# Performance work log

Hardware: AMD Instinct MI355X
Metric: run time of the kernel (lower is better)

The kernel has to match this reference:

```python
import jax, jax.numpy as jnp
import numpy as np

B = 8; R = 32; BS = 4; C = 128; H = 4; MLP = 512
SHIFT = BS // 2
N = BS ** 3            # tokens per window = 64
G = R // BS            # windows per axis = 8
NW = G ** 3            # windows per sample = 512
HD = C // H


def _rel_pos_index():
    # Faithful to the torch code: only coord 0 is scaled by (3*BS-1),
    # coords 1 and 2 are just added (index collisions are intentional here).
    coords = np.stack(np.meshgrid(np.arange(BS), np.arange(BS), np.arange(BS), indexing='ij'))
    cf = coords.reshape(3, -1)
    rel = (cf[:, :, None] - cf[:, None, :]).transpose(1, 2, 0).astype(np.int64)
    rel += BS - 1
    rel[:, :, 0] *= 3 * BS - 1
    return rel.sum(-1)  # (N, N)


def _attn_mask():
    img = np.zeros((R, R, R), np.float32)
    slices = (slice(0, -BS), slice(-BS, -SHIFT), slice(-SHIFT, None))
    cnt = 0
    for sx in slices:
        for sy in slices:
            for sz in slices:
                img[sx, sy, sz] = cnt
                cnt += 1
    boxes = img.reshape(G, BS, G, BS, G, BS).transpose(0, 2, 4, 1, 3, 5).reshape(-1, N)
    d = boxes[:, None, :] - boxes[:, :, None]  # (NW, N, N)
    return np.where(d != 0, np.float32(-100.0), np.float32(0.0))


_RPI = _rel_pos_index()
_MASK = _attn_mask()


def setup_inputs() -> dict:
    key = jax.random.key(0)
    ks = jax.random.split(key, 16)
    s = 0.02
    return {
        'inputs': jax.random.normal(ks[0], (B, R ** 3, C), jnp.float32),
        'qkv_w': jax.random.normal(ks[1], (C, 3 * C), jnp.float32) * s,
        'proj_w': jax.random.normal(ks[2], (C, C), jnp.float32) * s,
        'proj_b': jnp.zeros((C,), jnp.float32),
        'bias_table': jax.random.normal(ks[3], ((3 * BS - 1) ** 2, H), jnp.float32) * s,
        'g1': jnp.ones((C,), jnp.float32),
        'b1': jnp.zeros((C,), jnp.float32),
        'g2': jnp.ones((C,), jnp.float32),
        'b2': jnp.zeros((C,), jnp.float32),
        'w1': jax.random.normal(ks[4], (C, MLP), jnp.float32) * s,
        'bb1': jnp.zeros((MLP,), jnp.float32),
        'w2': jax.random.normal(ks[5], (MLP, C), jnp.float32) * s,
        'bb2': jnp.zeros((C,), jnp.float32),
    }


def _ln(x, g, b):
    m = x.mean(-1, keepdims=True)
    v = x.var(-1, keepdims=True)
    return (x - m) * jax.lax.rsqrt(v + 1e-5) * g + b


def reference(inputs, qkv_w, proj_w, proj_b, bias_table, g1, b1, g2, b2, w1, bb1, w2, bb2):
    rpi = jnp.asarray(_RPI)
    mask = jnp.asarray(_MASK)

    x = _ln(inputs, g1, b1).reshape(B, R, R, R, C)
    x = jnp.roll(x, (-SHIFT, -SHIFT, -SHIFT), axis=(1, 2, 3))
    # box partition -> (B*NW, N, C)
    boxes = x.reshape(B, G, BS, G, BS, G, BS, C).transpose(0, 1, 3, 5, 2, 4, 6, 7).reshape(-1, N, C)

    qkv = (boxes @ qkv_w).reshape(-1, N, 3, H, HD).transpose(2, 0, 3, 1, 4)
    q, k, v = qkv[0] * (HD ** -0.5), qkv[1], qkv[2]
    attn = jnp.einsum('bhnd,bhmd->bhnm', q, k)

    bias = bias_table[rpi.reshape(-1)].reshape(N, N, H).transpose(2, 0, 1)  # (H, N, N)
    attn = attn + bias[None]
    attn = attn.reshape(B, NW, H, N, N) + mask[None, :, None]
    attn = jax.nn.softmax(attn.reshape(-1, H, N, N), axis=-1)

    out = jnp.einsum('bhnm,bhmd->bhnd', attn, v).transpose(0, 2, 1, 3).reshape(-1, N, C)
    out = out @ proj_w + proj_b

    # box reverse + unshift
    out = out.reshape(B, G, G, G, BS, BS, BS, C).transpose(0, 1, 4, 2, 5, 3, 6, 7).reshape(B, R, R, R, C)
    out = jnp.roll(out, (SHIFT, SHIFT, SHIFT), axis=(1, 2, 3)).reshape(B, R ** 3, C)

    x = out * 0.5 + inputs
    h = _ln(x, g2, b2)
    h = jax.nn.gelu(h @ w1 + bb1, approximate=False) @ w2 + bb2
    return h * 0.5 + x
```

## Files before the change

kernel.cpp:

```cpp
#include <hip/hip_runtime.h>
#include <hip/hip_bf16.h>

typedef unsigned short u16;
typedef unsigned int u32;
typedef __attribute__((ext_vector_type(8))) short short8;
typedef __attribute__((ext_vector_type(4))) float f32x4;

__device__ __forceinline__ u16 f2bf(float x) {
  __hip_bfloat16 h = __float2bfloat16(x);
  return *reinterpret_cast<u16*>(&h);
}

__global__ void k_wprep(const float* __restrict__ src, u16* __restrict__ dst, int K, int N) {
  int idx = blockIdx.x * 256 + threadIdx.x;
  if (idx >= K * N) return;
  int k = idx / N, n = idx - k * N;
  dst[n * K + k] = f2bf(src[idx]);
}

__global__ __launch_bounds__(256, 2) void k_fused(const float* __restrict__ inputs,
                                                  const u16* __restrict__ qkvT,
                                                  const u16* __restrict__ projT,
                                                  const float* __restrict__ proj_b,
                                                  const float* __restrict__ btab,
                                                  const float* __restrict__ g1,
                                                  const float* __restrict__ b1,
                                                  float* __restrict__ xws) {
  __shared__ __align__(16) char lds[76800];
  u16* A_s  = (u16*)lds;
  u16* Q_s  = (u16*)(lds + 19456);
  u16* K_s  = (u16*)(lds + 36864);
  u16* P_s  = (u16*)lds;
  u16* O_s  = (u16*)(lds + 36864);
  u16* Vt_s = (u16*)(lds + 54272);
  float* bias_s = (float*)(lds + 72704);
  float* red    = (float*)(lds + 74752);

  const int t = threadIdx.x, wv = t >> 6, lane = t & 63;
  const int m = lane & 15, q4 = lane >> 4;
  const int bw = blockIdx.x;
  const int wbox = bw & 511, bsm = bw >> 9;
  const int gx = wbox >> 6, gy = (wbox >> 3) & 7, gz = wbox & 7;

  for (int i = t; i < 484; i += 256) bias_s[(i & 3) * 128 + (i >> 2)] = btab[i];

  short8 bq[4][2];
  #pragma unroll
  for (int kc = 0; kc < 4; ++kc)
    #pragma unroll
    for (int nt2 = 0; nt2 < 2; ++nt2)
      bq[kc][nt2] = *(const short8*)(qkvT + (size_t)(wv * 32 + nt2 * 16 + m) * 128 + kc * 32 + q4 * 8);

  {
    const int r1 = t >> 2, seg = t & 3;
    const int ix = r1 >> 4, iy = (r1 >> 2) & 3, iz = r1 & 3;
    const int X = (gx * 4 + ix + 2) & 31, Y = (gy * 4 + iy + 2) & 31, Z = (gz * 4 + iz + 2) & 31;
    const size_t orig = ((size_t)bsm << 15) + (size_t)(X * 1024 + Y * 32 + Z);
    const float4* x4 = (const float4*)(inputs + orig * 128 + seg * 32);
    float vals[32];
    float s = 0.f, ss = 0.f;
    #pragma unroll
    for (int i = 0; i < 8; ++i) {
      float4 v = x4[i];
      vals[4 * i] = v.x; vals[4 * i + 1] = v.y; vals[4 * i + 2] = v.z; vals[4 * i + 3] = v.w;
      s += v.x + v.y + v.z + v.w;
      ss += v.x * v.x + v.y * v.y + v.z * v.z + v.w * v.w;
    }
    red[r1 * 8 + seg] = s; red[r1 * 8 + 4 + seg] = ss;
    float sum = red[r1 * 8 + 0] + red[r1 * 8 + 1] + red[r1 * 8 + 2] + red[r1 * 8 + 3];
    float sq  = red[r1 * 8 + 4] + red[r1 * 8 + 5] + red[r1 * 8 + 6] + red[r1 * 8 + 7];
    float mean = sum * 0.0078125f;
    float var = sq * 0.0078125f - mean * mean;
    float rs = rsqrtf(var + 1e-5f);
    #pragma unroll
    for (int i = 0; i < 32; ++i) {
      int c = seg * 32 + i;
      A_s[r1 * 152 + c] = f2bf((vals[i] - mean) * rs * g1[c] + b1[c]);
    }
  }
  __syncthreads();

  short8 bk[4][2];
  #pragma unroll
  for (int kc = 0; kc < 4; ++kc)
    #pragma unroll
    for (int nt2 = 0; nt2 < 2; ++nt2)
      bk[kc][nt2] = *(const short8*)(qkvT + (size_t)(128 + wv * 32 + nt2 * 16 + m) * 128 + kc * 32 + q4 * 8);

  short8 af[4][4];
  #pragma unroll
  for (int kc = 0; kc < 4; ++kc)
    #pragma unroll
    for (int mt = 0; mt < 4; ++mt)
      af[kc][mt] = *(const short8*)(A_s + (mt * 16 + m) * 152 + kc * 32 + q4 * 8);

  f32x4 zero = {0.f, 0.f, 0.f, 0.f};

  {
    f32x4 acc1[4][2];
    #pragma unroll
    for (int mt = 0; mt < 4; ++mt)
      #pragma unroll
      for (int nt2 = 0; nt2 < 2; ++nt2) acc1[mt][nt2] = zero;
    #pragma unroll
    for (int kc = 0; kc < 4; ++kc)
      #pragma unroll
      for (int mt = 0; mt < 4; ++mt)
        #pragma unroll
        for (int nt2 = 0; nt2 < 2; ++nt2)
          acc1[mt][nt2] = __builtin_amdgcn_mfma_f32_16x16x32_bf16(af[kc][mt], bq[kc][nt2], acc1[mt][nt2], 0, 0, 0);
    #pragma unroll
    for (int mt = 0; mt < 4; ++mt)
      #pragma unroll
      for (int nt2 = 0; nt2 < 2; ++nt2)
        #pragma unroll
        for (int r = 0; r < 4; ++r)
          Q_s[(mt * 16 + q4 * 4 + r) * 136 + wv * 32 + nt2 * 16 + m] =
              f2bf(acc1[mt][nt2][r] * 0.17677669529663687f);
  }

  short8 bv[4][2];
  #pragma unroll
  for (int kc = 0; kc < 4; ++kc)
    #pragma unroll
    for (int nt2 = 0; nt2 < 2; ++nt2)
      bv[kc][nt2] = *(const short8*)(qkvT + (size_t)(256 + wv * 32 + nt2 * 16 + m) * 128 + kc * 32 + q4 * 8);

  {
    f32x4 acc1[4][2];
    #pragma unroll
    for (int mt = 0; mt < 4; ++mt)
      #pragma unroll
      for (int nt2 = 0; nt2 < 2; ++nt2) acc1[mt][nt2] = zero;
    #pragma unroll
    for (int kc = 0; kc < 4; ++kc)
      #pragma unroll
      for (int mt = 0; mt < 4; ++mt)
        #pragma unroll
        for (int nt2 = 0; nt2 < 2; ++nt2)
          acc1[mt][nt2] = __builtin_amdgcn_mfma_f32_16x16x32_bf16(af[kc][mt], bk[kc][nt2], acc1[mt][nt2], 0, 0, 0);
    #pragma unroll
    for (int mt = 0; mt < 4; ++mt)
      #pragma unroll
      for (int nt2 = 0; nt2 < 2; ++nt2)
        #pragma unroll
        for (int r = 0; r < 4; ++r)
          K_s[(mt * 16 + q4 * 4 + r) * 136 + wv * 32 + nt2 * 16 + m] = f2bf(acc1[mt][nt2][r]);
  }

  {
    f32x4 acc1[4][2];
    #pragma unroll
    for (int mt = 0; mt < 4; ++mt)
      #pragma unroll
      for (int nt2 = 0; nt2 < 2; ++nt2) acc1[mt][nt2] = zero;
    #pragma unroll
    for (int kc = 0; kc < 4; ++kc)
      #pragma unroll
      for (int mt = 0; mt < 4; ++mt)
        #pragma unroll
        for (int nt2 = 0; nt2 < 2; ++nt2)
          acc1[mt][nt2] = __builtin_amdgcn_mfma_f32_16x16x32_bf16(af[kc][mt], bv[kc][nt2], acc1[mt][nt2], 0, 0, 0);
    #pragma unroll
    for (int mt = 0; mt < 4; ++mt)
      #pragma unroll
      for (int nt2 = 0; nt2 < 2; ++nt2)
        #pragma unroll
        for (int r = 0; r < 4; ++r)
          Vt_s[wv * 2304 + (nt2 * 16 + m) * 72 + mt * 16 + q4 * 4 + r] = f2bf(acc1[mt][nt2][r]);
  }

  short8 qf[4], kf[4];
  #pragma unroll
  for (int ti = 0; ti < 4; ++ti) {
    qf[ti] = *(const short8*)(Q_s + (ti * 16 + m) * 136 + wv * 32 + q4 * 8);
    kf[ti] = *(const short8*)(K_s + (ti * 16 + m) * 136 + wv * 32 + q4 * 8);
  }
  __syncthreads();

  f32x4 S[4][4];
  #pragma unroll
  for (int ti = 0; ti < 4; ++ti)
    #pragma unroll
    for (int tj = 0; tj < 4; ++tj) S[ti][tj] = zero;
  #pragma unroll
  for (int ti = 0; ti < 4; ++ti)
    #pragma unroll
    for (int tj = 0; tj < 4; ++tj)
      S[ti][tj] = __builtin_amdgcn_mfma_f32_16x16x32_bf16(qf[ti], kf[tj], S[ti][tj], 0, 0, 0);

  int catx[4], caty[4], catz[4];
  #pragma unroll
  for (int a = 0; a < 4; ++a) {
    catx[a] = (gx < 7) ? 0 : ((a < 2) ? 1 : 2);
    caty[a] = (gy < 7) ? 0 : ((a < 2) ? 1 : 2);
    catz[a] = (gz < 7) ? 0 : ((a < 2) ? 1 : 2);
  }
  const int cy = (m >> 2) & 3, cz = m & 3;
  int labc[4], labr[16];
  #pragma unroll
  for (int tj = 0; tj < 4; ++tj) labc[tj] = catx[tj] * 9 + caty[cy] * 3 + catz[cz];
  #pragma unroll
  for (int ti = 0; ti < 4; ++ti)
    #pragma unroll
    for (int r = 0; r < 4; ++r) labr[ti * 4 + r] = catx[ti] * 9 + caty[q4] * 3 + catz[r];

  #pragma unroll
  for (int ti = 0; ti < 4; ++ti)
    #pragma unroll
    for (int tj = 0; tj < 4; ++tj) {
      int K0 = 11 * (ti - tj + 3) + (q4 + 3 - cy) + (3 - cz);
      #pragma unroll
      for (int r = 0; r < 4; ++r) {
        float v = S[ti][tj][r] + bias_s[wv * 128 + K0 + r];
        if (labr[ti * 4 + r] != labc[tj]) v -= 100.f;
        S[ti][tj][r] = v;
      }
    }

  float mx[16], sm[16];
  #pragma unroll
  for (int ti = 0; ti < 4; ++ti)
    #pragma unroll
    for (int r = 0; r < 4; ++r)
      mx[ti * 4 + r] = fmaxf(fmaxf(S[ti][0][r], S[ti][1][r]), fmaxf(S[ti][2][r], S[ti][3][r]));
  #pragma unroll
  for (int off = 1; off < 16; off <<= 1)
    #pragma unroll
    for (int i = 0; i < 16; ++i) mx[i] = fmaxf(mx[i], __shfl_xor(mx[i], off, 64));
  #pragma unroll
  for (int ti = 0; ti < 4; ++ti)
    #pragma unroll
    for (int r = 0; r < 4; ++r) {
      float e0 = __expf(S[ti][0][r] - mx[ti * 4 + r]);
      float e1 = __expf(S[ti][1][r] - mx[ti * 4 + r]);
      float e2 = __expf(S[ti][2][r] - mx[ti * 4 + r]);
      float e3 = __expf(S[ti][3][r] - mx[ti * 4 + r]);
      S[ti][0][r] = e0; S[ti][1][r] = e1; S[ti][2][r] = e2; S[ti][3][r] = e3;
      sm[ti * 4 + r] = (e0 + e1) + (e2 + e3);
    }
  #pragma unroll
  for (int off = 1; off < 16; off <<= 1)
    #pragma unroll
    for (int i = 0; i < 16; ++i) sm[i] += __shfl_xor(sm[i], off, 64);
  #pragma unroll
  for (int i = 0; i < 16; ++i) sm[i] = 1.f / sm[i];

  #pragma unroll
  for (int ti = 0; ti < 4; ++ti)
    #pragma unroll
    for (int tj = 0; tj < 4; ++tj)
      #pragma unroll
      for (int r = 0; r < 4; ++r)
        P_s[wv * 4608 + (ti * 16 + q4 * 4 + r) * 72 + tj * 16 + m] = f2bf(S[ti][tj][r]);

  f32x4 O[4][2];
  #pragma unroll
  for (int ti = 0; ti < 4; ++ti)
    #pragma unroll
    for (int tv = 0; tv < 2; ++tv) O[ti][tv] = zero;
  #pragma unroll
  for (int ks = 0; ks < 2; ++ks) {
    short8 pa[4], vb[2];
    #pragma unroll
    for (int ti = 0; ti < 4; ++ti)
      pa[ti] = *(const short8*)(P_s + wv * 4608 + (ti * 16 + m) * 72 + ks * 32 + q4 * 8);
    #pragma unroll
    for (int tv = 0; tv < 2; ++tv)
      vb[tv] = *(const short8*)(Vt_s + wv * 2304 + (tv * 16 + m) * 72 + ks * 32 + q4 * 8);
    #pragma unroll
    for (int ti = 0; ti < 4; ++ti)
      #pragma unroll
      for (int tv = 0; tv < 2; ++tv)
        O[ti][tv] = __builtin_amdgcn_mfma_f32_16x16x32_bf16(pa[ti], vb[tv], O[ti][tv], 0, 0, 0);
  }

  #pragma unroll
  for (int ti = 0; ti < 4; ++ti)
    #pragma unroll
    for (int tv = 0; tv < 2; ++tv)
      #pragma unroll
      for (int r = 0; r < 4; ++r)
        O_s[(ti * 16 + q4 * 4 + r) * 136 + wv * 32 + tv * 16 + m] = f2bf(O[ti][tv][r] * sm[ti * 4 + r]);

  short8 bp[4][2];
  #pragma unroll
  for (int kc = 0; kc < 4; ++kc)
    #pragma unroll
    for (int nt2 = 0; nt2 < 2; ++nt2)
      bp[kc][nt2] = *(const short8*)(projT + (size_t)(wv * 32 + nt2 * 16 + m) * 128 + kc * 32 + q4 * 8);
  float pb[2] = {proj_b[wv * 32 + m], proj_b[wv * 32 + 16 + m]};

  __syncthreads();

  short8 af2[4][4];
  #pragma unroll
  for (int kc = 0; kc < 4; ++kc)
    #pragma unroll
    for (int mt = 0; mt < 4; ++mt)
      af2[kc][mt] = *(const short8*)(O_s + (mt * 16 + m) * 136 + kc * 32 + q4 * 8);
  f32x4 acc2[4][2];
  #pragma unroll
  for (int mt = 0; mt < 4; ++mt)
    #pragma unroll
    for (int nt2 = 0; nt2 < 2; ++nt2) acc2[mt][nt2] = zero;
  #pragma unroll
  for (int kc = 0; kc < 4; ++kc)
    #pragma unroll
    for (int mt = 0; mt < 4; ++mt)
      #pragma unroll
      for (int nt2 = 0; nt2 < 2; ++nt2)
        acc2[mt][nt2] = __builtin_amdgcn_mfma_f32_16x16x32_bf16(af2[kc][mt], bp[kc][nt2], acc2[mt][nt2], 0, 0, 0);

  #pragma unroll
  for (int mt = 0; mt < 4; ++mt)
    #pragma unroll
    for (int r = 0; r < 4; ++r) {
      int nn = mt * 16 + q4 * 4 + r;
      int ix = nn >> 4, iy = (nn >> 2) & 3, iz = nn & 3;
      int X = (gx * 4 + ix + 2) & 31, Y = (gy * 4 + iy + 2) & 31, Z = (gz * 4 + iz + 2) & 31;
      size_t orig = ((size_t)bsm << 15) + (size_t)(X * 1024 + Y * 32 + Z);
      #pragma unroll
      for (int nt2 = 0; nt2 < 2; ++nt2) {
        int col = wv * 32 + nt2 * 16 + m;
        float v = acc2[mt][nt2][r] + pb[nt2];
        xws[orig * 128 + col] = 0.5f * v + inputs[orig * 128 + col];
      }
    }
}

__global__ __launch_bounds__(256, 2) void k_mlp(const float* __restrict__ x,
                                                const u16* __restrict__ w1T,
                                                const u16* __restrict__ w2T,
                                                const float* __restrict__ g2,
                                                const float* __restrict__ b2,
                                                const float* __restrict__ bb1,
                                                const float* __restrict__ bb2,
                                                float* __restrict__ out) {
  __shared__ __align__(16) char lds[19456];
  u16* A_s = (u16*)lds;
  float* red = (float*)(lds + 17408);
  u16* H0  = (u16*)lds;
  u16* H1  = (u16*)(lds + 9216);

  const int t = threadIdx.x, wid = t >> 6, lane = t & 63;
  const int m = lane & 15, q4 = lane >> 4;
  const size_t mbase = (size_t)blockIdx.x * 64;

  const u16* w1base = w1T + (size_t)(wid * 16 + m) * 128 + q4 * 8;
  short8 b1p0[4], b1p1[4];
  #pragma unroll
  for (int kc = 0; kc < 4; ++kc) b1p0[kc] = *(const short8*)(w1base + kc * 32);
  #pragma unroll
  for (int kc = 0; kc < 4; ++kc) b1p1[kc] = *(const short8*)(w1base + (size_t)64 * 128 + kc * 32);

  float bias1[8];
  #pragma unroll
  for (int nt = 0; nt < 8; ++nt) bias1[nt] = bb1[nt * 64 + wid * 16 + m];

  {
    int r1 = t >> 2, seg = t & 3;
    const float4* x4 = (const float4*)(x + (mbase + r1) * 128 + seg * 32);
    float vals[32];
    float s = 0.f, ss = 0.f;
    #pragma unroll
    for (int i = 0; i < 8; ++i) {
      float4 v = x4[i];
      vals[4 * i] = v.x; vals[4 * i + 1] = v.y; vals[4 * i + 2] = v.z; vals[4 * i + 3] = v.w;
      s += v.x + v.y + v.z + v.w;
      ss += v.x * v.x + v.y * v.y + v.z * v.z + v.w * v.w;
    }
    red[r1 * 8 + seg] = s; red[r1 * 8 + 4 + seg] = ss;
    float sum = red[r1 * 8 + 0] + red[r1 * 8 + 1] + red[r1 * 8 + 2] + red[r1 * 8 + 3];
    float sq  = red[r1 * 8 + 4] + red[r1 * 8 + 5] + red[r1 * 8 + 6] + red[r1 * 8 + 7];
    float mean = sum * 0.0078125f;
    float var = sq * 0.0078125f - mean * mean;
    float rs = rsqrtf(var + 1e-5f);
    #pragma unroll
    for (int i = 0; i < 32; ++i) {
      int c = seg * 32 + i;
      A_s[r1 * 136 + c] = f2bf((vals[i] - mean) * rs * g2[c] + b2[c]);
    }
  }
  __syncthreads();

  short8 af[4][4];
  #pragma unroll
  for (int kc = 0; kc < 4; ++kc)
    #pragma unroll
    for (int mt = 0; mt < 4; ++mt)
      af[kc][mt] = *(const short8*)(A_s + (mt * 16 + m) * 136 + kc * 32 + q4 * 8);
  __syncthreads();

  f32x4 zero = {0.f, 0.f, 0.f, 0.f};
  f32x4 acc[4][2];
  #pragma unroll
  for (int mt = 0; mt < 4; ++mt)
    #pragma unroll
    for (int nt2 = 0; nt2 < 2; ++nt2) acc[mt][nt2] = zero;

  #pragma unroll
  for (int nt = 0; nt < 8; ++nt) {
    u16* Hb = (nt & 1) ? H1 : H0;
    f32x4 hacc[4];
    #pragma unroll
    for (int mt = 0; mt < 4; ++mt) hacc[mt] = zero;
    if (nt & 1) {
      #pragma unroll
      for (int kc = 0; kc < 4; ++kc)
        #pragma unroll
        for (int mt = 0; mt < 4; ++mt)
          hacc[mt] = __builtin_amdgcn_mfma_f32_16x16x32_bf16(af[kc][mt], b1p1[kc], hacc[mt], 0, 0, 0);
    } else {
      #pragma unroll
      for (int kc = 0; kc < 4; ++kc)
        #pragma unroll
        for (int mt = 0; mt < 4; ++mt)
          hacc[mt] = __builtin_amdgcn_mfma_f32_16x16x32_bf16(af[kc][mt], b1p0[kc], hacc[mt], 0, 0, 0);
    }

    short8 b2f[2][2];
    #pragma unroll
    for (int kc2 = 0; kc2 < 2; ++kc2)
      #pragma unroll
      for (int nt2 = 0; nt2 < 2; ++nt2)
        b2f[kc2][nt2] = *(const short8*)(w2T + (size_t)(wid * 32 + nt2 * 16 + m) * 512 +
                                         nt * 64 + kc2 * 32 + q4 * 8);

    float bias = bias1[nt];
    #pragma unroll
    for (int mt = 0; mt < 4; ++mt)
      #pragma unroll
      for (int r = 0; r < 4; ++r) {
        float v = hacc[mt][r] + bias;
        float v2 = v * v;
        float qe = v * __builtin_fmaf(-0.07135482f, v2, -1.5957691f);
        float te = __expf(qe);
        float gl = v * __builtin_amdgcn_rcpf(1.f + te);
        Hb[(mt * 16 + q4 * 4 + r) * 72 + wid * 16 + m] = f2bf(gl);
      }
    __syncthreads();

    if (nt < 6) {
      const u16* p = w1base + (size_t)(nt + 2) * 64 * 128;
      if (nt & 1) {
        #pragma unroll
        for (int kc = 0; kc < 4; ++kc) b1p1[kc] = *(const short8*)(p + kc * 32);
      } else {
        #pragma unroll
        for (int kc = 0; kc < 4; ++kc) b1p0[kc] = *(const short8*)(p + kc * 32);
      }
    }

    #pragma unroll
    for (int kc2 = 0; kc2 < 2; ++kc2) {
      short8 a2[4];
      #pragma unroll
      for (int mt = 0; mt < 4; ++mt)
        a2[mt] = *(const short8*)(Hb + (mt * 16 + m) * 72 + kc2 * 32 + q4 * 8);
      #pragma unroll
      for (int mt = 0; mt < 4; ++mt)
        #pragma unroll
        for (int nt2 = 0; nt2 < 2; ++nt2)
          acc[mt][nt2] = __builtin_amdgcn_mfma_f32_16x16x32_bf16(a2[mt], b2f[kc2][nt2],
                                                                 acc[mt][nt2], 0, 0, 0);
    }
  }

  #pragma unroll
  for (int mt = 0; mt < 4; ++mt)
    #pragma unroll
    for (int nt2 = 0; nt2 < 2; ++nt2)
      #pragma unroll
      for (int r = 0; r < 4; ++r) {
        size_t tok = mbase + mt * 16 + q4 * 4 + r;
        int col = wid * 32 + nt2 * 16 + m;
        float v = acc[mt][nt2][r] + bb2[col];
        out[tok * 128 + col] = 0.5f * v + x[tok * 128 + col];
      }
}

extern "C" void kernel_launch(void* const* d_in, const int* in_sizes, int n_in,
                              void* d_out, int out_size, void* d_ws, size_t ws_size,
                              hipStream_t stream) {
  const float* inputs = (const float*)d_in[0];
  const float* qkv_w  = (const float*)d_in[1];
  const float* proj_w = (const float*)d_in[2];
  const float* proj_b = (const float*)d_in[3];
  const float* btab   = (const float*)d_in[4];
  const float* g1     = (const float*)d_in[5];
  const float* b1     = (const float*)d_in[6];
  const float* g2     = (const float*)d_in[7];
  const float* b2     = (const float*)d_in[8];
  const float* w1     = (const float*)d_in[9];
  const float* bb1    = (const float*)d_in[10];
  const float* w2     = (const float*)d_in[11];
  const float* bb2    = (const float*)d_in[12];
  float* out = (float*)d_out;

  char* ws = (char*)d_ws;
  u16* qkvT  = (u16*)(ws + 0);
  u16* projT = (u16*)(ws + 98304);
  u16* w1T   = (u16*)(ws + 131072);
  u16* w2T   = (u16*)(ws + 262144);
  float* xws = (float*)(ws + 393216);

  k_wprep<<<192, 256, 0, stream>>>(qkv_w, qkvT, 128, 384);
  k_wprep<<<64, 256, 0, stream>>>(proj_w, projT, 128, 128);
  k_wprep<<<256, 256, 0, stream>>>(w1, w1T, 128, 512);
  k_wprep<<<256, 256, 0, stream>>>(w2, w2T, 512, 128);

  k_fused<<<4096, 256, 0, stream>>>(inputs, qkvT, projT, proj_b, btab, g1, b1, xws);
  k_mlp<<<4096, 256, 0, stream>>>(xws, w1T, w2T, g2, b2, bb1, bb2, out);
}
```

Baseline: 509.8 us.

## Fuse window attention and MLP into one kernel, merge weight prep launches

```diff
diff --git a/kernel.cpp b/kernel.cpp
--- a/kernel.cpp
+++ b/kernel.cpp
@@ -11,21 +11,47 @@
   return *reinterpret_cast<u16*>(&h);
 }
 
-__global__ void k_wprep(const float* __restrict__ src, u16* __restrict__ dst, int K, int N) {
-  int idx = blockIdx.x * 256 + threadIdx.x;
-  if (idx >= K * N) return;
-  int k = idx / N, n = idx - k * N;
-  dst[n * K + k] = f2bf(src[idx]);
+__global__ __launch_bounds__(256) void k_wprep4(const float* __restrict__ qkv_w,
+                                                const float* __restrict__ proj_w,
+                                                const float* __restrict__ w1,
+                                                const float* __restrict__ w2,
+                                                u16* __restrict__ qkvT, u16* __restrict__ projT,
+                                                u16* __restrict__ w1T, u16* __restrict__ w2T) {
+  __shared__ float tile[64][65];
+  const int b = blockIdx.x, t = threadIdx.x;
+  const float* src; u16* dst; int K, N, tk, tn;
+  if (b < 12)      { src = qkv_w;  dst = qkvT;  K = 128; N = 384; tk = b / 6;        tn = b % 6; }
+  else if (b < 16) { src = proj_w; dst = projT; K = 128; N = 128; tk = (b - 12) / 2; tn = (b - 12) % 2; }
+  else if (b < 32) { src = w1;     dst = w1T;   K = 128; N = 512; tk = (b - 16) / 8; tn = (b - 16) % 8; }
+  else             { src = w2;     dst = w2T;   K = 512; N = 128; tk = (b - 32) / 2; tn = (b - 32) % 2; }
+  const int rb = t >> 6, c = t & 63;
+  #pragma unroll
+  for (int i = 0; i < 16; ++i) {
+    int r = i * 4 + rb;
+    tile[r][c] = src[(size_t)(tk * 64 + r) * N + tn * 64 + c];
+  }
+  __syncthreads();
+  #pragma unroll
+  for (int i = 0; i < 16; ++i) {
+    int rr = i * 4 + rb;
+    dst[(size_t)(tn * 64 + rr) * K + tk * 64 + c] = f2bf(tile[c][rr]);
+  }
 }
 
-__global__ __launch_bounds__(256, 2) void k_fused(const float* __restrict__ inputs,
-                                                  const u16* __restrict__ qkvT,
-                                                  const u16* __restrict__ projT,
-                                                  const float* __restrict__ proj_b,
-                                                  const float* __restrict__ btab,
-                                                  const float* __restrict__ g1,
-                                                  const float* __restrict__ b1,
-                                                  float* __restrict__ xws) {
+__global__ __launch_bounds__(256, 2) void k_all(const float* __restrict__ inputs,
+                                                const u16* __restrict__ qkvT,
+                                                const u16* __restrict__ projT,
+                                                const float* __restrict__ proj_b,
+                                                const float* __restrict__ btab,
+                                                const float* __restrict__ g1,
+                                                const float* __restrict__ b1,
+                                                const u16* __restrict__ w1T,
+                                                const u16* __restrict__ w2T,
+                                                const float* __restrict__ g2,
+                                                const float* __restrict__ b2,
+                                                const float* __restrict__ bb1,
+                                                const float* __restrict__ bb2,
+                                                float* __restrict__ out) {
   __shared__ __align__(16) char lds[76800];
   u16* A_s  = (u16*)lds;
   u16* Q_s  = (u16*)(lds + 19456);
@@ -35,6 +61,10 @@
   u16* Vt_s = (u16*)(lds + 54272);
   float* bias_s = (float*)(lds + 72704);
   float* red    = (float*)(lds + 74752);
+  float* X_s = (float*)lds;
+  u16* A2_s  = (u16*)(lds + 36864);
+  u16* H0    = (u16*)(lds + 54272);
+  u16* H1    = (u16*)(lds + 63488);
 
   const int t = threadIdx.x, wv = t >> 6, lane = t & 63;
   const int m = lane & 15, q4 = lane >> 4;
@@ -315,60 +345,40 @@
   #pragma unroll
   for (int mt = 0; mt < 4; ++mt)
     #pragma unroll
-    for (int r = 0; r < 4; ++r) {
-      int nn = mt * 16 + q4 * 4 + r;
-      int ix = nn >> 4, iy = (nn >> 2) & 3, iz = nn & 3;
-      int X = (gx * 4 + ix + 2) & 31, Y = (gy * 4 + iy + 2) & 31, Z = (gz * 4 + iz + 2) & 31;
-      size_t orig = ((size_t)bsm << 15) + (size_t)(X * 1024 + Y * 32 + Z);
-      #pragma unroll
-      for (int nt2 = 0; nt2 < 2; ++nt2) {
-        int col = wv * 32 + nt2 * 16 + m;
-        float v = acc2[mt][nt2][r] + pb[nt2];
-        xws[orig * 128 + col] = 0.5f * v + inputs[orig * 128 + col];
-      }
-    }
-}
-
-__global__ __launch_bounds__(256, 2) void k_mlp(const float* __restrict__ x,
-                                                const u16* __restrict__ w1T,
-                                                const u16* __restrict__ w2T,
-                                                const float* __restrict__ g2,
-                                                const float* __restrict__ b2,
-                                                const float* __restrict__ bb1,
-                                                const float* __restrict__ bb2,
-                                                float* __restrict__ out) {
-  __shared__ __align__(16) char lds[19456];
-  u16* A_s = (u16*)lds;
-  float* red = (float*)(lds + 17408);
-  u16* H0  = (u16*)lds;
-  u16* H1  = (u16*)(lds + 9216);
-
-  const int t = threadIdx.x, wid = t >> 6, lane = t & 63;
-  const int m = lane & 15, q4 = lane >> 4;
-  const size_t mbase = (size_t)blockIdx.x * 64;
-
-  const u16* w1base = w1T + (size_t)(wid * 16 + m) * 128 + q4 * 8;
+    for (int nt2 = 0; nt2 < 2; ++nt2)
+      #pragma unroll
+      for (int r = 0; r < 4; ++r)
+        X_s[(mt * 16 + q4 * 4 + r) * 132 + wv * 32 + nt2 * 16 + m] = 0.5f * (acc2[mt][nt2][r] + pb[nt2]);
+
+  __syncthreads();
+
+  const u16* w1base = w1T + (size_t)(wv * 16 + m) * 128 + q4 * 8;
   short8 b1p0[4], b1p1[4];
   #pragma unroll
   for (int kc = 0; kc < 4; ++kc) b1p0[kc] = *(const short8*)(w1base + kc * 32);
   #pragma unroll
   for (int kc = 0; kc < 4; ++kc) b1p1[kc] = *(const short8*)(w1base + (size_t)64 * 128 + kc * 32);
-
   float bias1[8];
   #pragma unroll
-  for (int nt = 0; nt < 8; ++nt) bias1[nt] = bb1[nt * 64 + wid * 16 + m];
+  for (int nt = 0; nt < 8; ++nt) bias1[nt] = bb1[nt * 64 + wv * 16 + m];
 
   {
-    int r1 = t >> 2, seg = t & 3;
-    const float4* x4 = (const float4*)(x + (mbase + r1) * 128 + seg * 32);
+    const int r1 = t >> 2, seg = t & 3;
+    const int ix = r1 >> 4, iy = (r1 >> 2) & 3, iz = r1 & 3;
+    const int X = (gx * 4 + ix + 2) & 31, Y = (gy * 4 + iy + 2) & 31, Z = (gz * 4 + iz + 2) & 31;
+    const size_t orig = ((size_t)bsm << 15) + (size_t)(X * 1024 + Y * 32 + Z);
+    const float4* x4 = (const float4*)(inputs + orig * 128 + seg * 32);
     float vals[32];
     float s = 0.f, ss = 0.f;
     #pragma unroll
     for (int i = 0; i < 8; ++i) {
       float4 v = x4[i];
-      vals[4 * i] = v.x; vals[4 * i + 1] = v.y; vals[4 * i + 2] = v.z; vals[4 * i + 3] = v.w;
-      s += v.x + v.y + v.z + v.w;
-      ss += v.x * v.x + v.y * v.y + v.z * v.z + v.w * v.w;
+      float* xp = X_s + r1 * 132 + seg * 32 + 4 * i;
+      float a0 = xp[0] + v.x, a1 = xp[1] + v.y, a2 = xp[2] + v.z, a3 = xp[3] + v.w;
+      xp[0] = a0; xp[1] = a1; xp[2] = a2; xp[3] = a3;
+      vals[4 * i] = a0; vals[4 * i + 1] = a1; vals[4 * i + 2] = a2; vals[4 * i + 3] = a3;
+      s += a0 + a1 + a2 + a3;
+      ss += a0 * a0 + a1 * a1 + a2 * a2 + a3 * a3;
     }
     red[r1 * 8 + seg] = s; red[r1 * 8 + 4 + seg] = ss;
     float sum = red[r1 * 8 + 0] + red[r1 * 8 + 1] + red[r1 * 8 + 2] + red[r1 * 8 + 3];
@@ -379,20 +389,18 @@
     #pragma unroll
     for (int i = 0; i < 32; ++i) {
       int c = seg * 32 + i;
-      A_s[r1 * 136 + c] = f2bf((vals[i] - mean) * rs * g2[c] + b2[c]);
+      A2_s[r1 * 136 + c] = f2bf((vals[i] - mean) * rs * g2[c] + b2[c]);
     }
   }
   __syncthreads();
 
-  short8 af[4][4];
-  #pragma unroll
-  for (int kc = 0; kc < 4; ++kc)
-    #pragma unroll
-    for (int mt = 0; mt < 4; ++mt)
-      af[kc][mt] = *(const short8*)(A_s + (mt * 16 + m) * 136 + kc * 32 + q4 * 8);
-  __syncthreads();
-
-  f32x4 zero = {0.f, 0.f, 0.f, 0.f};
+  short8 am[4][4];
+  #pragma unroll
+  for (int kc = 0; kc < 4; ++kc)
+    #pragma unroll
+    for (int mt = 0; mt < 4; ++mt)
+      am[kc][mt] = *(const short8*)(A2_s + (mt * 16 + m) * 136 + kc * 32 + q4 * 8);
+
   f32x4 acc[4][2];
   #pragma unroll
   for (int mt = 0; mt < 4; ++mt)
@@ -410,13 +418,13 @@
       for (int kc = 0; kc < 4; ++kc)
         #pragma unroll
         for (int mt = 0; mt < 4; ++mt)
-          hacc[mt] = __builtin_amdgcn_mfma_f32_16x16x32_bf16(af[kc][mt], b1p1[kc], hacc[mt], 0, 0, 0);
+          hacc[mt] = __builtin_amdgcn_mfma_f32_16x16x32_bf16(am[kc][mt], b1p1[kc], hacc[mt], 0, 0, 0);
     } else {
       #pragma unroll
       for (int kc = 0; kc < 4; ++kc)
         #pragma unroll
         for (int mt = 0; mt < 4; ++mt)
-          hacc[mt] = __builtin_amdgcn_mfma_f32_16x16x32_bf16(af[kc][mt], b1p0[kc], hacc[mt], 0, 0, 0);
+          hacc[mt] = __builtin_amdgcn_mfma_f32_16x16x32_bf16(am[kc][mt], b1p0[kc], hacc[mt], 0, 0, 0);
     }
 
     short8 b2f[2][2];
@@ -424,7 +432,7 @@
     for (int kc2 = 0; kc2 < 2; ++kc2)
       #pragma unroll
       for (int nt2 = 0; nt2 < 2; ++nt2)
-        b2f[kc2][nt2] = *(const short8*)(w2T + (size_t)(wid * 32 + nt2 * 16 + m) * 512 +
+        b2f[kc2][nt2] = *(const short8*)(w2T + (size_t)(wv * 32 + nt2 * 16 + m) * 512 +
                                          nt * 64 + kc2 * 32 + q4 * 8);
 
     float bias = bias1[nt];
@@ -437,7 +445,7 @@
         float qe = v * __builtin_fmaf(-0.07135482f, v2, -1.5957691f);
         float te = __expf(qe);
         float gl = v * __builtin_amdgcn_rcpf(1.f + te);
-        Hb[(mt * 16 + q4 * 4 + r) * 72 + wid * 16 + m] = f2bf(gl);
+        Hb[(mt * 16 + q4 * 4 + r) * 72 + wv * 16 + m] = f2bf(gl);
       }
     __syncthreads();
 
@@ -467,17 +475,22 @@
     }
   }
 
+  float ob[2] = {bb2[wv * 32 + m], bb2[wv * 32 + 16 + m]};
   #pragma unroll
   for (int mt = 0; mt < 4; ++mt)
     #pragma unroll
-    for (int nt2 = 0; nt2 < 2; ++nt2)
-      #pragma unroll
-      for (int r = 0; r < 4; ++r) {
-        size_t tok = mbase + mt * 16 + q4 * 4 + r;
-        int col = wid * 32 + nt2 * 16 + m;
-        float v = acc[mt][nt2][r] + bb2[col];
-        out[tok * 128 + col] = 0.5f * v + x[tok * 128 + col];
+    for (int r = 0; r < 4; ++r) {
+      int nn = mt * 16 + q4 * 4 + r;
+      int ix = nn >> 4, iy = (nn >> 2) & 3, iz = nn & 3;
+      int X = (gx * 4 + ix + 2) & 31, Y = (gy * 4 + iy + 2) & 31, Z = (gz * 4 + iz + 2) & 31;
+      size_t orig = ((size_t)bsm << 15) + (size_t)(X * 1024 + Y * 32 + Z);
+      #pragma unroll
+      for (int nt2 = 0; nt2 < 2; ++nt2) {
+        int col = wv * 32 + nt2 * 16 + m;
+        float v = acc[mt][nt2][r] + ob[nt2];
+        out[orig * 128 + col] = 0.5f * v + X_s[nn * 132 + col];
       }
+    }
 }
 
 extern "C" void kernel_launch(void* const* d_in, const int* in_sizes, int n_in,
@@ -503,13 +516,8 @@
   u16* projT = (u16*)(ws + 98304);
   u16* w1T   = (u16*)(ws + 131072);
   u16* w2T   = (u16*)(ws + 262144);
-  float* xws = (float*)(ws + 393216);
-
-  k_wprep<<<192, 256, 0, stream>>>(qkv_w, qkvT, 128, 384);
-  k_wprep<<<64, 256, 0, stream>>>(proj_w, projT, 128, 128);
-  k_wprep<<<256, 256, 0, stream>>>(w1, w1T, 128, 512);
-  k_wprep<<<256, 256, 0, stream>>>(w2, w2T, 512, 128);
-
-  k_fused<<<4096, 256, 0, stream>>>(inputs, qkvT, projT, proj_b, btab, g1, b1, xws);
-  k_mlp<<<4096, 256, 0, stream>>>(xws, w1T, w2T, g2, b2, bb1, bb2, out);
+
+  k_wprep4<<<48, 256, 0, stream>>>(qkv_w, proj_w, w1, w2, qkvT, projT, w1T, w2T);
+  k_all<<<4096, 256, 0, stream>>>(inputs, qkvT, projT, proj_b, btab, g1, b1,
+                                  w1T, w2T, g2, b2, bb1, bb2, out);
 }
```

After: 481.7 us. 1.06x faster.
